# Optimization experiments

Measured on AMD Instinct MI355X. Metric: run time of the kernel, lower is better.

## Reference

```python
import jax, jax.numpy as jnp
import numpy as np

FS = 44100.0
TWO_PI = 2.0 * np.pi


def setup_inputs() -> dict:
    key = jax.random.key(0)
    ks = jax.random.split(key, 12)
    B, T, H, NF, NB = 4, 64000, 96, 4, 8
    f0 = jax.random.uniform(ks[0], (B, T, 1), minval=100.0, maxval=400.0)
    amplitudes = jax.random.uniform(ks[1], (B, T, H))
    vibrato_rate = 5.0 + jax.random.uniform(ks[2], (B, T, 1))
    vibrato_depth = 0.2 * jax.random.uniform(ks[3], (B, T, 1))
    ff = jnp.array([800.0, 1150.0, 2900.0, 3900.0], dtype=jnp.float32)
    fb = jnp.array([80.0, 90.0, 120.0, 130.0], dtype=jnp.float32)
    fg = jnp.array([1.0, 0.5, 0.25, 0.1], dtype=jnp.float32)
    formant_freqs = ff[None, None] * (0.9 + 0.2 * jax.random.uniform(ks[4], (B, T, NF)))
    formant_bandwidths = fb[None, None] * (0.9 + 0.2 * jax.random.uniform(ks[5], (B, T, NF)))
    formant_gains = fg[None, None] * (0.9 + 0.2 * jax.random.uniform(ks[6], (B, T, NF)))
    glottal_open_quotient = 0.5 + 0.4 * jax.random.uniform(ks[7], (B, T, 1))
    phase_coherence = jax.random.uniform(ks[8], (B, T, 1))
    breathiness = 0.3 * jax.random.uniform(ks[9], (B, T, 1))
    breath_spectral_shape = jax.random.uniform(ks[10], (B, T, NB))
    initial_phase = jnp.zeros((B, 1, 1), dtype=jnp.float32)
    return dict(f0=f0, amplitudes=amplitudes, vibrato_rate=vibrato_rate,
                vibrato_depth=vibrato_depth, formant_freqs=formant_freqs,
                formant_bandwidths=formant_bandwidths, formant_gains=formant_gains,
                glottal_open_quotient=glottal_open_quotient,
                phase_coherence=phase_coherence, breathiness=breathiness,
                breath_spectral_shape=breath_spectral_shape, initial_phase=initial_phase)


def _breath_noise(noise, spectral_weights):
    # noise: [B,T]; spectral_weights: [B,n_bands] (mid frame) -> normalized shaped noise [B,T]
    B, T = noise.shape
    n_bands = spectral_weights.shape[1]
    shaped = jnp.zeros_like(noise)
    for i in range(n_bands):  # small fixed band loop (structurally distinct kernel sizes)
        smooth = 2.0 ** (i / 2.0)
        ksz = max(3, int(128 / smooth))
        if ksz % 2 == 0:
            ksz += 1
        g = np.exp(-np.arange(-(ksz // 2), ksz // 2 + 1) ** 2 / (2.0 * (ksz / 6.0) ** 2))
        kern = jnp.asarray(g / g.sum(), dtype=jnp.float32)
        smoothed = jax.lax.conv_general_dilated(
            noise[:, None, :], kern[None, None, :], (1,), 'SAME')[:, 0, :]
        shaped = shaped + smoothed * spectral_weights[:, i:i + 1]
    mean = shaped.mean(axis=1, keepdims=True)
    std = shaped.std(axis=1, ddof=1, keepdims=True) + 1e-8
    return (shaped - mean) / std


def _forward(f0, amplitudes, vibrato_rate, vibrato_depth, formant_freqs,
             formant_bandwidths, formant_gains, glottal_open_quotient,
             phase_coherence, breathiness, breath_spectral_shape, initial_phase, noise):
    B, T, H = amplitudes.shape
    fs = FS
    # --- vibrato ---
    t = (jnp.arange(T, dtype=jnp.float32) / fs)[None, :, None]
    vib_factor = 2.0 ** (vibrato_depth / 12.0)
    vib_mult = jnp.exp(jnp.sin(TWO_PI * vibrato_rate * t) * jnp.log(vib_factor))
    f0_vib = jnp.where(f0 > 0, f0 * vib_mult, f0)  # B,T,1
    # --- per-harmonic phases via cumulative fundamental phase ---
    fund_phase = jnp.cumsum(TWO_PI * f0_vib / fs, axis=1) + initial_phase  # B,T,1
    n = jnp.arange(1, H + 1, dtype=jnp.float32)  # harmonic numbers
    phases = fund_phase * n  # B,T,H
    # --- phase coherence: blend higher harmonics toward n * fundamental ---
    coherent = fund_phase * n[1:]
    blended = phase_coherence * coherent + (1.0 - phase_coherence) * phases[:, :, 1:]
    phases = jnp.concatenate([phases[:, :, :1], blended], axis=2)
    # --- remove above Nyquist ---
    amp = jnp.where(f0_vib * n < fs / 2.0, amplitudes, jnp.zeros_like(amplitudes))
    # --- glottal flow model ---
    norm_phase = jnp.mod(phases, TWO_PI) / TWO_PI
    oq = glottal_open_quotient
    half_pi = jnp.float32(np.pi / 2.0)
    rising = jnp.sin(norm_phase / oq * half_pi) ** 2
    falling = jnp.cos((norm_phase - oq) / (1.0 - oq) * half_pi) ** 2
    flow = jnp.where(norm_phase < oq, rising, falling) - 0.5
    signal = jnp.sum(flow * amp, axis=-1)  # B,T
    # --- formant filter (mid-frame params, vectorized over batch & formants) ---
    mid = T // 2
    freqs = jnp.fft.rfftfreq(T, d=1.0 / fs).astype(jnp.float32)  # [F]
    fmid = formant_freqs[:, mid][:, :, None]       # B,NF,1
    bwmid = formant_bandwidths[:, mid][:, :, None]
    gmid = formant_gains[:, mid][:, :, None]
    resp = (gmid / (1.0 + ((freqs[None, None, :] - fmid) / (bwmid / 2.0)) ** 2)).sum(1)  # B,F
    filtered = jnp.fft.irfft(jnp.fft.rfft(signal) * resp, n=T)  # B,T
    # --- breath noise mix ---
    breath = _breath_noise(noise, breath_spectral_shape[:, mid])  # B,T
    br = breathiness[:, :, 0]
    out = filtered * (1.0 - br) + breath * br
    final_phase = jnp.mod(fund_phase[:, -1:, :], TWO_PI)  # B,1,1
    return out, final_phase


def reference(f0, amplitudes, vibrato_rate, vibrato_depth, formant_freqs,
              formant_bandwidths, formant_gains, glottal_open_quotient,
              phase_coherence, breathiness, breath_spectral_shape, initial_phase):
    B, T = f0.shape[0], f0.shape[1]
    noise = jax.random.normal(jax.random.key(42), (B, T), dtype=jnp.float32)
    return _forward(f0, amplitudes, vibrato_rate, vibrato_depth, formant_freqs,
                    formant_bandwidths, formant_gains, glottal_open_quotient,
                    phase_coherence, breathiness, breath_spectral_shape,
                    initial_phase, noise)
```

## Files before the change

kernel.cpp:

```cpp
#include <hip/hip_runtime.h>
#include <math.h>
#include <stdint.h>

#define B_ 4
#define T_ 64000
#define H_ 96
#define NCH 1000
#define TT_ 64
#define TWO_PI_D 6.283185307179586

typedef float2 cplx;
__device__ __forceinline__ cplx cadd(cplx a, cplx b){ return make_float2(a.x+b.x, a.y+b.y); }
__device__ __forceinline__ cplx csub(cplx a, cplx b){ return make_float2(a.x-b.x, a.y-b.y); }
__device__ __forceinline__ cplx cmul(cplx a, cplx b){ return make_float2(a.x*b.x - a.y*b.y, a.x*b.y + a.y*b.x); }

__device__ float  g_dpf[B_*T_];
__device__ unsigned char g_hcnt[B_*T_];
__device__ float  g_signal[B_*T_];
__device__ float  g_shaped[B_*T_];
__device__ float  g_Kcomb[B_][132];
__device__ float2 g_W1[2*512*125];
__device__ float2 g_Z[2*125*512];
__device__ double g_chunksum[B_*NCH];
__device__ double g_stats[B_*2];
__device__ double g_part[B_*NCH*2];

__device__ __forceinline__ double fsin64(double x){
  double z = x * 0.63661977236758138243;
  double fn = floor(z + 0.5);
  int k = (int)fn;
  const double p1 = 1.57079632673412561417e+00;
  const double p2 = 6.07710050650619224932e-11;
  double r = x - fn*p1;
  r = r - fn*p2;
  double s = r*r;
  double ps = 1.58969099521155010221e-10;
  ps = ps*s - 2.50507602534068634195e-08;
  ps = ps*s + 2.75573137070700676789e-06;
  ps = ps*s - 1.98412698298579493134e-04;
  ps = ps*s + 8.33333333332248946124e-03;
  ps = ps*s - 1.66666666666666324348e-01;
  double sr = r + r*s*ps;
  double pc = -1.13596475577881948265e-11;
  pc = pc*s + 2.08757232129817482790e-09;
  pc = pc*s - 2.75573143513906633035e-07;
  pc = pc*s + 2.48015872894767294178e-05;
  pc = pc*s - 1.38888888888741095749e-03;
  pc = pc*s + 4.16666666666666019037e-02;
  double cr = 1.0 - 0.5*s + s*s*pc;
  int m = k & 3;
  return (m==0) ? sr : (m==1) ? cr : (m==2) ? -sr : -cr;
}

__device__ __forceinline__ double fexp_small(double x){
  double p = 1.9841269841269841e-04;
  p = p*x + 1.3888888888888889e-03;
  p = p*x + 8.3333333333333332e-03;
  p = p*x + 4.1666666666666664e-02;
  p = p*x + 1.6666666666666666e-01;
  p = p*x + 0.5;
  p = p*x + 1.0;
  p = p*x + 1.0;
  return p;
}

__device__ __forceinline__ uint32_t rotl32(uint32_t x, int r){ return (x<<r)|(x>>(32-r)); }

__device__ __forceinline__ uint32_t threefry_bits(uint32_t i){
  uint32_t x0 = 0u, x1 = i;
  const uint32_t ks0 = 0u, ks1 = 42u, ks2 = 0u ^ 42u ^ 0x1BD11BDAu;
  x0 += ks0; x1 += ks1;
  #define TFR(r) { x0 += x1; x1 = rotl32(x1, r); x1 ^= x0; }
  TFR(13) TFR(15) TFR(26) TFR(6)   x0 += ks1; x1 += ks2 + 1u;
  TFR(17) TFR(29) TFR(16) TFR(24)  x0 += ks2; x1 += ks0 + 2u;
  TFR(13) TFR(15) TFR(26) TFR(6)   x0 += ks0; x1 += ks1 + 3u;
  TFR(17) TFR(29) TFR(16) TFR(24)  x0 += ks1; x1 += ks2 + 4u;
  TFR(13) TFR(15) TFR(26) TFR(6)   x0 += ks2; x1 += ks0 + 5u;
  #undef TFR
  return x0 ^ x1;
}

__device__ __forceinline__ float bits_to_normal(uint32_t bits){
  uint32_t mbits = (bits >> 9) | 0x3F800000u;
  float f = __uint_as_float(mbits) - 1.0f;
  const float lo = -0.99999994f;
  float x = f * 2.0f + lo;
  x = fmaxf(lo, x);
  float w = -log1pf(-x*x);
  float p;
  if (w < 5.0f){
    w -= 2.5f;
    p = 2.81022636e-08f;
    p = fmaf(p, w, 3.43273939e-07f);
    p = fmaf(p, w, -3.5233877e-06f);
    p = fmaf(p, w, -4.39150654e-06f);
    p = fmaf(p, w, 0.00021858087f);
    p = fmaf(p, w, -0.00125372503f);
    p = fmaf(p, w, -0.00417768164f);
    p = fmaf(p, w, 0.246640727f);
    p = fmaf(p, w, 1.50140941f);
  } else {
    w = sqrtf(w) - 3.0f;
    p = -0.000200214257f;
    p = fmaf(p, w, 0.000100950558f);
    p = fmaf(p, w, 0.00134934322f);
    p = fmaf(p, w, -0.00367342844f);
    p = fmaf(p, w, 0.00573950773f);
    p = fmaf(p, w, -0.0076224613f);
    p = fmaf(p, w, 0.00943887047f);
    p = fmaf(p, w, 1.00167406f);
    p = fmaf(p, w, 2.83297682f);
  }
  return 1.4142135623730951f * (p * x);
}

__constant__ int KSZc[8] = {129,91,65,45,33,23,17,11};

__global__ __launch_bounds__(256) void k_phase(const float* __restrict__ bss,
                                               const float* __restrict__ f0,
                                               const float* __restrict__ vr,
                                               const float* __restrict__ vd){
  int b = blockIdx.x / 250, c = blockIdx.x % 250;
  int t0 = c*256, tid = threadIdx.x;
  if (c == 0){
    __shared__ float wn[8];
    {
      int i = tid >> 5, l32 = tid & 31;
      int ksz = KSZc[i];
      float sig = (float)ksz / 6.0f;
      float inv2s2 = 1.0f/(2.0f*sig*sig);
      int ctr = ksz>>1;
      float s = 0.f;
      for (int j = l32; j < ksz; j += 32){
        float d = (float)(j - ctr);
        s += expf(-d*d*inv2s2);
      }
      #pragma unroll
      for (int o=1;o<32;o<<=1) s += __shfl_xor(s, o);
      if (l32 == 0) wn[i] = bss[((size_t)b*T_ + T_/2)*8 + i] / s;
    }
    __syncthreads();
    if (tid < 129){
      int tau = tid - 64;
      float acc = 0.f;
      #pragma unroll
      for (int i=0;i<8;i++){
        int ksz = KSZc[i]; int hw = ksz>>1;
        if (tau >= -hw && tau <= hw){
          float sig = (float)ksz/6.0f;
          float inv2s2 = 1.0f/(2.0f*sig*sig);
          acc += expf(-(float)(tau*tau)*inv2s2) * wn[i];
        }
      }
      g_Kcomb[b][tid] = acc;
    }
  }
  int t = t0 + tid;
  int idx = b*T_ + t;
  double tt = (double)t * 2.2675736961451248e-05;
  double argd = TWO_PI_D * (double)vr[idx] * tt;
  double argr = argd - TWO_PI_D * floor(argd * 0.15915494309189535);
  float svf = __sinf((float)argr);
  double lm = (double)vd[idx] * 0.057762265046662105;
  double vm = fexp_small((double)svf * lm);
  double f0s = (double)f0[idx];
  double f0v = (f0s > 0.0) ? f0s * vm : f0s;
  int cnt;
  if (f0v <= 0.0) cnt = 96;
  else {
    int n = (int)(22050.0f / (float)f0v);
    if (!((double)n * f0v < 22050.0)) n--;
    if ((double)(n+1) * f0v < 22050.0) n++;
    double dlo = 22050.0 - (double)n * f0v;
    double dhi = (double)(n+1) * f0v - 22050.0;
    if (dlo < 0.01 || dhi < 0.01){
      double sv_d = fsin64(argd);
      double vm_d = fexp_small(sv_d * lm);
      double f0x = f0s * vm_d;
      int n2 = (int)(22050.0f / (float)f0x);
      if (!((double)n2 * f0x < 22050.0)) n2--;
      if ((double)(n2+1) * f0x < 22050.0) n2++;
      n = n2;
      f0v = f0x;
    }
    cnt = (n < 0) ? 0 : ((n > 96) ? 96 : n);
  }
  g_hcnt[idx] = (unsigned char)cnt;
  double v = f0v * 1.4247585730565955e-04;
  g_dpf[idx] = (float)v;
  int lane = tid & 63, wid = tid >> 6;
  for (int o=1;o<64;o<<=1) v += __shfl_down(v, o);
  if (lane == 0) g_chunksum[b*NCH + c*4 + wid] = v;
}

__global__ __launch_bounds__(256) void k_sigbreath(const float* __restrict__ amps,
                                                   const float* __restrict__ goq,
                                                   const float* __restrict__ iph,
                                                   float* __restrict__ out_final){
  __shared__ float ph[TT_];
  __shared__ float ns[192];
  __shared__ float kl[132];
  __shared__ float shb[TT_];
  int b = blockIdx.x / NCH, c = blockIdx.x % NCH;
  int t0 = c*TT_;
  int tid = threadIdx.x;
  int tl = tid >> 2, part = tid & 3;
  const float4* Ar = (const float4*)(amps + ((size_t)b*T_ + t0 + tl)*H_ + part*24);
  float4 a0 = Ar[0], a1 = Ar[1], a2 = Ar[2], a3 = Ar[3], a4 = Ar[4], a5 = Ar[5];
  int idx = b*T_ + t0 + tl;
  int hc = (int)g_hcnt[idx];
  float oq = goq[idx];
  if (tid < 64){
    double s = 0.0;
    for (int ch = tid; ch < c; ch += 64) s += g_chunksum[b*NCH + ch];
    for (int o=1;o<64;o<<=1) s += __shfl_xor(s, o);
    double base = s + (double)iph[b];
    int idq = b*T_ + t0 + tid;
    double v = (double)g_dpf[idq];
    for (int o=1;o<64;o<<=1){ double u = __shfl_up(v, o); if (tid >= o) v += u; }
    ph[tid] = (float)fmod(base + v, TWO_PI_D);
    if (c == NCH-1 && tid == 63) out_final[b] = (float)fmod(base + v, TWO_PI_D);
  }
  {
    int k = (tid < 64) ? tid + 128 : tid - 64;
    int t = t0 - 64 + k;
    float nv = 0.f;
    if (t >= 0 && t < T_) nv = bits_to_normal(threefry_bits((uint32_t)(b*T_ + t)));
    if (k < 192) ns[k] = nv;
  }
  if (tid >= 192){
    for (int k = tid - 192; k < 129; k += 64) kl[k] = g_Kcomb[b][k];
  }
  __syncthreads();
  {
    float accb = 0.f;
    for (int j = part; j < 129; j += 4) accb = fmaf(ns[tl + j], kl[j], accb);
    accb += __shfl_xor(accb, 1);
    accb += __shfl_xor(accb, 2);
    if (part == 0) shb[tl] = accb;
  }
  float r = ph[tl];
  float k1 = 3.14159265358979f / oq;
  float k2 = 3.14159265358979f / (1.0f - oq);
  float offA = 3.14159265358979f;
  float offB = -oq * k2;
  float r0 = r * 0.15915494309189535f;
  int hbase = part*24;
  float sum = 0.f;
  float av[24] = {a0.x,a0.y,a0.z,a0.w, a1.x,a1.y,a1.z,a1.w, a2.x,a2.y,a2.z,a2.w,
                  a3.x,a3.y,a3.z,a3.w, a4.x,a4.y,a4.z,a4.w, a5.x,a5.y,a5.z,a5.w};
  #pragma unroll
  for (int e=0;e<24;e++){
    int h = hbase + e;
    float amp = (h < hc) ? av[e] : 0.0f;
    float nn = (float)(h+1);
    float fr = nn * r0;
    fr = fr - floorf(fr);
    bool ris = fr < oq;
    float kk  = ris ? k1 : k2;
    float off = ris ? offA : offB;
    float cv = __cosf(fmaf(fr, kk, off));
    sum = fmaf(cv, amp, sum);
  }
  sum += __shfl_xor(sum, 1);
  sum += __shfl_xor(sum, 2);
  if (part == 0) g_signal[idx] = 0.5f * sum;
  __syncthreads();
  if (tid < 64){
    float sv = shb[tid];
    g_shaped[b*T_ + t0 + tid] = sv;
    double xx = (double)sv;
    double s1 = xx, s2 = xx*xx;
    for (int o=1;o<64;o<<=1){ s1 += __shfl_down(s1,o); s2 += __shfl_down(s2,o); }
    if (tid == 0){
      g_part[(b*NCH+c)*2]   = s1;
      g_part[(b*NCH+c)*2+1] = s2;
    }
  }
}

template<int SGN>
__device__ __forceinline__ float2* fft512_r4(float2* bufA, float2* bufB, int tid){
  float2* src = bufA; float2* dst = bufB;
  #pragma unroll
  for (int st=0; st<4; st++){
    const int s = 1<<(2*st);
    const int n = 512>>(2*st);
    const int m = n>>2;
    if (tid < 128){
      int p = tid / s;
      int q = tid - p*s;
      float2 a0 = src[q + s*p];
      float2 a1 = src[q + s*(p+m)];
      float2 a2 = src[q + s*(p+2*m)];
      float2 a3 = src[q + s*(p+3*m)];
      float2 t0 = cadd(a0,a2), t1 = csub(a0,a2);
      float2 t2 = cadd(a1,a3), t3 = csub(a1,a3);
      float2 it3 = make_float2(-(float)SGN*t3.y, (float)SGN*t3.x);
      float2 r0 = cadd(t0,t2);
      float2 r1 = cadd(t1,it3);
      float2 r2 = csub(t0,t2);
      float2 r3 = csub(t1,it3);
      float ba = (float)SGN * ((float)(2.0*M_PI)/(float)n) * (float)p;
      dst[q + s*(4*p+0)] = r0;
      float sw,cw;
      __sincosf(ba, &sw, &cw);
      dst[q + s*(4*p+1)] = cmul(make_float2(cw,sw), r1);
      __sincosf(2.f*ba, &sw, &cw);
      dst[q + s*(4*p+2)] = cmul(make_float2(cw,sw), r2);
      __sincosf(3.f*ba, &sw, &cw);
      dst[q + s*(4*p+3)] = cmul(make_float2(cw,sw), r3);
    }
    __syncthreads();
    float2* tp = src; src = dst; dst = tp;
  }
  {
    float2 a = src[tid];
    float2 bb = src[tid+256];
    dst[tid]     = cadd(a,bb);
    dst[tid+256] = csub(a,bb);
    __syncthreads();
    float2* tp = src; src = dst; dst = tp;
  }
  return src;
}

__device__ __forceinline__ cplx w5k(int k, float sgn){
  const float C[5] = {1.f, 0.30901699f, -0.80901699f, -0.80901699f, 0.30901699f};
  const float S[5] = {0.f, 0.95105652f, 0.58778525f, -0.58778525f, -0.95105652f};
  return make_float2(C[k], sgn*S[k]);
}

template<int SGN>
__device__ __forceinline__ float2* fft125_rows(float2* bufA, float2* bufB, int tid){
  float2* src = bufA; float2* dst = bufB;
  #pragma unroll
  for (int st=0; st<3; st++){
    const int s = (st==0)?1:((st==1)?5:25);
    const int n = (st==0)?125:((st==1)?25:5);
    const int m = n/5;
    if (tid < 200){
      int row = tid/25, w = tid - row*25;
      int p = w/s, q = w - p*s;
      int base = row*125 + q;
      float2 a0 = src[base + s*p];
      float2 a1 = src[base + s*(p+m)];
      float2 a2 = src[base + s*(p+2*m)];
      float2 a3 = src[base + s*(p+3*m)];
      float2 a4 = src[base + s*(p+4*m)];
      #pragma unroll
      for (int r2=0;r2<5;r2++){
        float2 acc = a0;
        acc = cadd(acc, cmul(a1, w5k((1*r2)%5, (float)SGN)));
        acc = cadd(acc, cmul(a2, w5k((2*r2)%5, (float)SGN)));
        acc = cadd(acc, cmul(a3, w5k((3*r2)%5, (float)SGN)));
        acc = cadd(acc, cmul(a4, w5k((4*r2)%5, (float)SGN)));
        float ang = (float)SGN * ((float)(2.0*M_PI)/(float)n) * (float)(p*r2);
        float sw,cw; __sincosf(ang,&sw,&cw);
        dst[base + s*(5*p+r2)] = cmul(make_float2(cw,sw), acc);
      }
    }
    __syncthreads();
    float2* tp = src; src = dst; dst = tp;
  }
  return src;
}

__global__ __launch_bounds__(256) void k_fft512_fwd(){
  int p = blockIdx.x / 125, n1 = blockIdx.x % 125;
  int tid = threadIdx.x;
  __shared__ float2 bufA[512];
  __shared__ float2 bufB[512];
  const float* sa = g_signal + (size_t)(2*p)*T_;
  const float* sb = g_signal + (size_t)(2*p+1)*T_;
  for (int i=tid;i<512;i+=256) bufA[i] = make_float2(sa[n1 + 125*i], sb[n1 + 125*i]);
  __syncthreads();
  float2* res = fft512_r4<-1>(bufA, bufB, tid);
  for (int i=tid;i<512;i+=256){
    float ang = -(float)(2.0*M_PI/64000.0) * (float)(n1*i);
    float sw,cw; __sincosf(ang,&sw,&cw);
    g_W1[((size_t)p*512 + i)*125 + n1] = cmul(make_float2(cw,sw), res[i]);
  }
  if (blockIdx.x < B_){
    int b = blockIdx.x;
    double s1=0.0, s2=0.0;
    if (tid < 250){
      #pragma unroll
      for (int k=0;k<4;k++){
        int ch = tid*4 + k;
        s1 += g_part[(b*NCH+ch)*2];
        s2 += g_part[(b*NCH+ch)*2+1];
      }
    }
    for (int o=1;o<64;o<<=1){ s1 += __shfl_down(s1,o); s2 += __shfl_down(s2,o); }
    __shared__ double a1[4], a2[4];
    int lane = tid&63, wid = tid>>6;
    if (lane==0){ a1[wid]=s1; a2[wid]=s2; }
    __syncthreads();
    if (tid==0){
      double S1=a1[0]+a1[1]+a1[2]+a1[3], S2=a2[0]+a2[1]+a2[2]+a2[3];
      double mean = S1 / (double)T_;
      double var = (S2 - (double)T_*mean*mean) / (double)(T_-1);
      if (var < 0.0) var = 0.0;
      double rstd = 1.0/(sqrt(var) + 1e-8);
      g_stats[b*2] = mean; g_stats[b*2+1] = rstd;
    }
  }
}

__global__ __launch_bounds__(256) void k_fft125_mid(const float* __restrict__ ffq,
                                                    const float* __restrict__ fbw,
                                                    const float* __restrict__ fgn){
  int p = blockIdx.x / 64;
  int j = blockIdx.x % 64;
  int tid = threadIdx.x;
  __shared__ float2 bufA[1000];
  __shared__ float2 bufB[1000];
  int k2r[8];
  #pragma unroll
  for (int l=0;l<8;l++){
    int k2;
    if (l < 4) k2 = 4*j + l;
    else if (j==0 && l==4) k2 = 256;
    else k2 = 512 - 4*j - (l-4);
    k2r[l] = k2;
  }
  for (int i=tid;i<1000;i+=256){
    int l = i/125, n1 = i - l*125;
    bufA[i] = g_W1[((size_t)p*512 + k2r[l])*125 + n1];
  }
  float fca[4], bwa[4], ga[4], fcb[4], bwb[4], gb[4];
  int ba = 2*p, bb = 2*p+1;
  #pragma unroll
  for (int q=0;q<4;q++){
    size_t ia = ((size_t)ba*T_ + T_/2)*4 + q;
    size_t ib = ((size_t)bb*T_ + T_/2)*4 + q;
    fca[q]=ffq[ia]; bwa[q]=fbw[ia]; ga[q]=fgn[ia];
    fcb[q]=ffq[ib]; bwb[q]=fbw[ib]; gb[q]=fgn[ib];
  }
  __syncthreads();
  float2* X = fft125_rows<-1>(bufA, bufB, tid);
  float2* Y = (X == bufA) ? bufB : bufA;
  for (int i=tid;i<1000;i+=256){
    int l = i/125, k1 = i - l*125;
    int k2 = k2r[l];
    int lm = ((j==0) && (l==0 || l==4)) ? l : (l^4);
    int k1m = (k2 == 0) ? ((k1==0)?0:(125-k1)) : (124-k1);
    float2 Z1 = X[l*125 + k1];
    float2 Z2 = X[lm*125 + k1m];
    float xax = 0.5f*(Z1.x + Z2.x), xay = 0.5f*(Z1.y - Z2.y);
    float xbx = 0.5f*(Z1.y + Z2.y), xby = -0.5f*(Z1.x - Z2.x);
    int f = k2 + 512*k1;
    int fi = (f <= 32000) ? f : (64000 - f);
    float freq = (float)fi * 0.6890625f;
    float ra = 0.f, rb = 0.f;
    #pragma unroll
    for (int q=0;q<4;q++){
      float da = (freq - fca[q]) / (bwa[q]*0.5f);
      ra += ga[q] / (1.0f + da*da);
      float db = (freq - fcb[q]) / (bwb[q]*0.5f);
      rb += gb[q] / (1.0f + db*db);
    }
    float yax = ra*xax, yay = ra*xay;
    float ybx = rb*xbx, yby = rb*xby;
    Y[i] = make_float2(yax - yby, yay + ybx);
  }
  __syncthreads();
  float2* res2 = fft125_rows<1>(Y, X, tid);
  for (int i=tid;i<1000;i+=256){
    int l = i/125, n1 = i - l*125;
    int k2 = k2r[l];
    float ang = (float)(2.0*M_PI/64000.0) * (float)(n1*k2);
    float sw,cw; __sincosf(ang,&sw,&cw);
    g_Z[((size_t)p*125 + n1)*512 + k2] = cmul(make_float2(cw,sw), res2[i]);
  }
}

__global__ __launch_bounds__(256) void k_fft512_inv(const float* __restrict__ brth,
                                                    float* __restrict__ outp){
  int p = blockIdx.x / 125, n1 = blockIdx.x % 125;
  int tid = threadIdx.x;
  __shared__ float2 bufA[512];
  __shared__ float2 bufB[512];
  const float2* gin = g_Z + ((size_t)p*125 + n1)*512;
  for (int i=tid;i<512;i+=256) bufA[i] = gin[i];
  __syncthreads();
  float2* res = fft512_r4<1>(bufA, bufB, tid);
  int ba = 2*p, bb = 2*p+1;
  float mean_a = (float)g_stats[ba*2], rstd_a = (float)g_stats[ba*2+1];
  float mean_b = (float)g_stats[bb*2], rstd_b = (float)g_stats[bb*2+1];
  for (int i=tid;i<512;i+=256){
    int t = n1 + 125*i;
    float2 v = res[i];
    {
      int idx = ba*T_ + t;
      float filt = v.x * (1.0f/64000.0f);
      float br = brth[idx];
      float breath = (g_shaped[idx] - mean_a) * rstd_a;
      outp[idx] = filt*(1.0f - br) + breath*br;
    }
    {
      int idx = bb*T_ + t;
      float filt = v.y * (1.0f/64000.0f);
      float br = brth[idx];
      float breath = (g_shaped[idx] - mean_b) * rstd_b;
      outp[idx] = filt*(1.0f - br) + breath*br;
    }
  }
}

extern "C" void kernel_launch(void* const* d_in, const int* in_sizes, int n_in,
                              void* d_out, int out_size, void* d_ws, size_t ws_size,
                              hipStream_t stream){
  (void)in_sizes; (void)n_in; (void)out_size; (void)d_ws; (void)ws_size;
  const float* f0   = (const float*)d_in[0];
  const float* amps = (const float*)d_in[1];
  const float* vr   = (const float*)d_in[2];
  const float* vd   = (const float*)d_in[3];
  const float* ffq  = (const float*)d_in[4];
  const float* fbw  = (const float*)d_in[5];
  const float* fgn  = (const float*)d_in[6];
  const float* goq  = (const float*)d_in[7];
  const float* brth = (const float*)d_in[9];
  const float* bss  = (const float*)d_in[10];
  const float* iph  = (const float*)d_in[11];
  float* out = (float*)d_out;
  float* out_final = out + (size_t)B_*T_;

  k_phase<<<B_*250,256,0,stream>>>(bss, f0, vr, vd);
  k_sigbreath<<<B_*NCH,256,0,stream>>>(amps, goq, iph, out_final);
  k_fft512_fwd<<<250,256,0,stream>>>();
  k_fft125_mid<<<128,256,0,stream>>>(ffq, fbw, fgn);
  k_fft512_inv<<<250,256,0,stream>>>(brth, out);
}
```

Measured before the change: 61.62 us.

## Split breath-noise convolution into dedicated blocks interleaved with synthesis blocks

```diff
diff --git a/kernel.cpp b/kernel.cpp
--- a/kernel.cpp
+++ b/kernel.cpp
@@ -23,7 +23,7 @@
 __device__ float2 g_Z[2*125*512];
 __device__ double g_chunksum[B_*NCH];
 __device__ double g_stats[B_*2];
-__device__ double g_part[B_*NCH*2];
+__device__ double g_part[B_*250*2];
 
 __device__ __forceinline__ double fsin64(double x){
   double z = x * 0.63661977236758138243;
@@ -193,89 +193,89 @@
   if (lane == 0) g_chunksum[b*NCH + c*4 + wid] = v;
 }
 
-__global__ __launch_bounds__(256) void k_sigbreath(const float* __restrict__ amps,
-                                                   const float* __restrict__ goq,
-                                                   const float* __restrict__ iph,
-                                                   float* __restrict__ out_final){
-  __shared__ float ph[TT_];
-  __shared__ float ns[192];
-  __shared__ float kl[132];
-  __shared__ float shb[TT_];
-  int b = blockIdx.x / NCH, c = blockIdx.x % NCH;
-  int t0 = c*TT_;
+__global__ __launch_bounds__(256) void k_synth(const float* __restrict__ amps,
+                                               const float* __restrict__ goq,
+                                               const float* __restrict__ iph,
+                                               float* __restrict__ out_final){
+  __shared__ float sh_ns[384];
+  __shared__ float sh_kl[132];
+  __shared__ float sh_ph[TT_];
+  __shared__ double sh_red[8];
+  int bid = blockIdx.x;
   int tid = threadIdx.x;
-  int tl = tid >> 2, part = tid & 3;
-  const float4* Ar = (const float4*)(amps + ((size_t)b*T_ + t0 + tl)*H_ + part*24);
-  float4 a0 = Ar[0], a1 = Ar[1], a2 = Ar[2], a3 = Ar[3], a4 = Ar[4], a5 = Ar[5];
-  int idx = b*T_ + t0 + tl;
-  int hc = (int)g_hcnt[idx];
-  float oq = goq[idx];
-  if (tid < 64){
-    double s = 0.0;
-    for (int ch = tid; ch < c; ch += 64) s += g_chunksum[b*NCH + ch];
-    for (int o=1;o<64;o<<=1) s += __shfl_xor(s, o);
-    double base = s + (double)iph[b];
-    int idq = b*T_ + t0 + tid;
-    double v = (double)g_dpf[idq];
-    for (int o=1;o<64;o<<=1){ double u = __shfl_up(v, o); if (tid >= o) v += u; }
-    ph[tid] = (float)fmod(base + v, TWO_PI_D);
-    if (c == NCH-1 && tid == 63) out_final[b] = (float)fmod(base + v, TWO_PI_D);
-  }
-  {
-    int k = (tid < 64) ? tid + 128 : tid - 64;
-    int t = t0 - 64 + k;
-    float nv = 0.f;
-    if (t >= 0 && t < T_) nv = bits_to_normal(threefry_bits((uint32_t)(b*T_ + t)));
-    if (k < 192) ns[k] = nv;
-  }
-  if (tid >= 192){
-    for (int k = tid - 192; k < 129; k += 64) kl[k] = g_Kcomb[b][k];
-  }
-  __syncthreads();
-  {
-    float accb = 0.f;
-    for (int j = part; j < 129; j += 4) accb = fmaf(ns[tl + j], kl[j], accb);
-    accb += __shfl_xor(accb, 1);
-    accb += __shfl_xor(accb, 2);
-    if (part == 0) shb[tl] = accb;
-  }
-  float r = ph[tl];
-  float k1 = 3.14159265358979f / oq;
-  float k2 = 3.14159265358979f / (1.0f - oq);
-  float offA = 3.14159265358979f;
-  float offB = -oq * k2;
-  float r0 = r * 0.15915494309189535f;
-  int hbase = part*24;
-  float sum = 0.f;
-  float av[24] = {a0.x,a0.y,a0.z,a0.w, a1.x,a1.y,a1.z,a1.w, a2.x,a2.y,a2.z,a2.w,
-                  a3.x,a3.y,a3.z,a3.w, a4.x,a4.y,a4.z,a4.w, a5.x,a5.y,a5.z,a5.w};
-  #pragma unroll
-  for (int e=0;e<24;e++){
-    int h = hbase + e;
-    float amp = (h < hc) ? av[e] : 0.0f;
-    float nn = (float)(h+1);
-    float fr = nn * r0;
-    fr = fr - floorf(fr);
-    bool ris = fr < oq;
-    float kk  = ris ? k1 : k2;
-    float off = ris ? offA : offB;
-    float cv = __cosf(fmaf(fr, kk, off));
-    sum = fmaf(cv, amp, sum);
-  }
-  sum += __shfl_xor(sum, 1);
-  sum += __shfl_xor(sum, 2);
-  if (part == 0) g_signal[idx] = 0.5f * sum;
-  __syncthreads();
-  if (tid < 64){
-    float sv = shb[tid];
-    g_shaped[b*T_ + t0 + tid] = sv;
-    double xx = (double)sv;
+  if ((bid % 5) == 4){
+    int bb = bid / 5;
+    int b = bb / 250, c = bb % 250;
+    int t0 = c * 256;
+    for (int k = tid; k < 384; k += 256){
+      int t = t0 - 64 + k;
+      float nv = 0.f;
+      if (t >= 0 && t < T_) nv = bits_to_normal(threefry_bits((uint32_t)(b*T_ + t)));
+      sh_ns[k] = nv;
+    }
+    for (int k = tid; k < 129; k += 256) sh_kl[k] = g_Kcomb[b][k];
+    __syncthreads();
+    float acc = 0.f;
+    for (int j = 0; j < 129; j++) acc = fmaf(sh_ns[tid + j], sh_kl[j], acc);
+    g_shaped[b*T_ + t0 + tid] = acc;
+    double xx = (double)acc;
     double s1 = xx, s2 = xx*xx;
     for (int o=1;o<64;o<<=1){ s1 += __shfl_down(s1,o); s2 += __shfl_down(s2,o); }
-    if (tid == 0){
-      g_part[(b*NCH+c)*2]   = s1;
-      g_part[(b*NCH+c)*2+1] = s2;
-    }
+    int lane = tid&63, wid = tid>>6;
+    if (lane==0){ sh_red[wid] = s1; sh_red[4+wid] = s2; }
+    __syncthreads();
+    if (tid==0){
+      g_part[(b*250+c)*2]   = sh_red[0]+sh_red[1]+sh_red[2]+sh_red[3];
+      g_part[(b*250+c)*2+1] = sh_red[4]+sh_red[5]+sh_red[6]+sh_red[7];
+    }
+  } else {
+    int sb = bid - bid/5;
+    int b = sb / NCH, c = sb % NCH;
+    int t0 = c * TT_;
+    int tl = tid >> 2, part = tid & 3;
+    const float4* Ar = (const float4*)(amps + ((size_t)b*T_ + t0 + tl)*H_ + part*24);
+    float4 a0 = Ar[0], a1 = Ar[1], a2 = Ar[2], a3 = Ar[3], a4 = Ar[4], a5 = Ar[5];
+    int idx = b*T_ + t0 + tl;
+    int hc = (int)g_hcnt[idx];
+    float oq = goq[idx];
+    if (tid < 64){
+      double s = 0.0;
+      for (int ch = tid; ch < c; ch += 64) s += g_chunksum[b*NCH + ch];
+      for (int o=1;o<64;o<<=1) s += __shfl_xor(s, o);
+      double base = s + (double)iph[b];
+      int idq = b*T_ + t0 + tid;
+      double v = (double)g_dpf[idq];
+      for (int o=1;o<64;o<<=1){ double u = __shfl_up(v, o); if (tid >= o) v += u; }
+      sh_ph[tid] = (float)fmod(base + v, TWO_PI_D);
+      if (c == NCH-1 && tid == 63) out_final[b] = (float)fmod(base + v, TWO_PI_D);
+    }
+    __syncthreads();
+    float r = sh_ph[tl];
+    float k1 = 3.14159265358979f / oq;
+    float k2 = 3.14159265358979f / (1.0f - oq);
+    float offA = 3.14159265358979f;
+    float offB = -oq * k2;
+    float r0 = r * 0.15915494309189535f;
+    int hbase = part*24;
+    float sum = 0.f;
+    float av[24] = {a0.x,a0.y,a0.z,a0.w, a1.x,a1.y,a1.z,a1.w, a2.x,a2.y,a2.z,a2.w,
+                    a3.x,a3.y,a3.z,a3.w, a4.x,a4.y,a4.z,a4.w, a5.x,a5.y,a5.z,a5.w};
+    #pragma unroll
+    for (int e=0;e<24;e++){
+      int h = hbase + e;
+      float amp = (h < hc) ? av[e] : 0.0f;
+      float nn = (float)(h+1);
+      float fr = nn * r0;
+      fr = fr - floorf(fr);
+      bool ris = fr < oq;
+      float kk  = ris ? k1 : k2;
+      float off = ris ? offA : offB;
+      float cv = __cosf(fmaf(fr, kk, off));
+      sum = fmaf(cv, amp, sum);
+    }
+    sum += __shfl_xor(sum, 1);
+    sum += __shfl_xor(sum, 2);
+    if (part == 0) g_signal[idx] = 0.5f * sum;
   }
 }
 
@@ -384,14 +384,7 @@
   if (blockIdx.x < B_){
     int b = blockIdx.x;
     double s1=0.0, s2=0.0;
-    if (tid < 250){
-      #pragma unroll
-      for (int k=0;k<4;k++){
-        int ch = tid*4 + k;
-        s1 += g_part[(b*NCH+ch)*2];
-        s2 += g_part[(b*NCH+ch)*2+1];
-      }
-    }
+    if (tid < 250){ s1 = g_part[(b*250+tid)*2]; s2 = g_part[(b*250+tid)*2+1]; }
     for (int o=1;o<64;o<<=1){ s1 += __shfl_down(s1,o); s2 += __shfl_down(s2,o); }
     __shared__ double a1[4], a2[4];
     int lane = tid&63, wid = tid>>6;
@@ -528,7 +521,7 @@
   float* out_final = out + (size_t)B_*T_;
 
   k_phase<<<B_*250,256,0,stream>>>(bss, f0, vr, vd);
-  k_sigbreath<<<B_*NCH,256,0,stream>>>(amps, goq, iph, out_final);
+  k_synth<<<5000,256,0,stream>>>(amps, goq, iph, out_final);
   k_fft512_fwd<<<250,256,0,stream>>>();
   k_fft125_mid<<<128,256,0,stream>>>(ffq, fbw, fgn);
   k_fft512_inv<<<250,256,0,stream>>>(brth, out);
```

Measured after the change: 56.02 us, median of 2. 1.1x faster.
